# Kernel tuning notes

Hardware: AMD Instinct MI355X
Metric: run time of the kernel (lower is better)

## Reference

```python
import jax, jax.numpy as jnp
import numpy as np

T, N, E = 4, 50000, 800000
F, H, C_HID, C_OUT = 256, 128, 512, 2
SLOPE = 11.0 / 48.0  # torch RReLU eval-mode slope = (1/8 + 1/3) / 2


def _topk_pool(x, scorer, k):
    # x: [N, d], scorer: [d, 1] -> [d, k]
    scores = (x @ scorer) / jnp.maximum(jnp.linalg.norm(scorer), 1e-6)  # [N, 1]
    _, idx = jax.lax.top_k(scores[:, 0], k)
    return (x[idx] * jnp.tanh(scores[idx])).T


def _gru_cell(prev_Q, z, Wu, Uu, bu, Wr, Ur, br, Wh, Uh, bh):
    u = jax.nn.sigmoid(Wu @ z + Uu @ prev_Q + bu)
    r = jax.nn.sigmoid(Wr @ z + Ur @ prev_Q + br)
    h_cap = jnp.tanh(Wh @ z + Uh @ (r * prev_Q) + bh)
    return (1.0 - u) * prev_Q + u * h_cap


def _gcn_conv(x, src, dst, W):
    ones = jnp.ones(src.shape[0], x.dtype)
    deg_out = jnp.clip(jax.ops.segment_sum(ones, src, num_segments=N), 1.0)
    deg_in = jnp.clip(jax.ops.segment_sum(ones, dst, num_segments=N), 1.0)
    h = (x * (deg_out ** -0.5)[:, None]) @ W          # project first (out <= in)
    agg = jax.ops.segment_sum(h[src], dst, num_segments=N)
    out = agg * (deg_in ** -0.5)[:, None]
    return jnp.where(out >= 0, out, SLOPE * out)      # RReLU (eval mode)


def setup_inputs() -> dict:
    key = jax.random.key(0)
    ks = jax.random.split(key, 32)
    s = 0.05
    d = {}
    d['feats'] = jax.random.normal(ks[0], (T, N, F), jnp.float32)
    d['edges'] = jax.random.randint(ks[1], (T, 2, E), 0, N)
    d['scorer0'] = jax.random.normal(ks[2], (F, 1), jnp.float32) * s
    d['scorer1'] = jax.random.normal(ks[3], (H, 1), jnp.float32) * s
    d['gcn_W0'] = jax.random.normal(ks[4], (F, H), jnp.float32) * s
    d['gcn_W1'] = jax.random.normal(ks[5], (H, H), jnp.float32) * s
    i = 6
    for g in ('u', 'r', 'h'):
        d[g + '_W0'] = jax.random.normal(ks[i], (F, F), jnp.float32) * s; i += 1
        d[g + '_U0'] = jax.random.normal(ks[i], (F, F), jnp.float32) * s; i += 1
        d[g + '_b0'] = jax.random.normal(ks[i], (F, H), jnp.float32) * s; i += 1
    for g in ('u', 'r', 'h'):
        d[g + '_W1'] = jax.random.normal(ks[i], (H, H), jnp.float32) * s; i += 1
        d[g + '_U1'] = jax.random.normal(ks[i], (H, H), jnp.float32) * s; i += 1
        d[g + '_b1'] = jax.random.normal(ks[i], (H, H), jnp.float32) * s; i += 1
    d['mlp_W1'] = jax.random.normal(ks[i], (H, C_HID), jnp.float32) * s; i += 1
    d['mlp_b1'] = jax.random.normal(ks[i], (C_HID,), jnp.float32) * s; i += 1
    d['mlp_W2'] = jax.random.normal(ks[i], (C_HID, C_OUT), jnp.float32) * s; i += 1
    d['mlp_b2'] = jax.random.normal(ks[i], (C_OUT,), jnp.float32) * s
    return d


def reference(feats, edges, scorer0, scorer1, gcn_W0, gcn_W1,
              u_W0, u_U0, u_b0, r_W0, r_U0, r_b0, h_W0, h_U0, h_b0,
              u_W1, u_U1, u_b1, r_W1, r_U1, r_b1, h_W1, h_U1, h_b1,
              mlp_W1, mlp_b1, mlp_W2, mlp_b2):
    feat_list = [feats[t] for t in range(T)]
    scorers = [scorer0, scorer1]
    gcn_Ws = [gcn_W0, gcn_W1]
    grus = [(u_W0, u_U0, u_b0, r_W0, r_U0, r_b0, h_W0, h_U0, h_b0),
            (u_W1, u_U1, u_b1, r_W1, r_U1, r_b1, h_W1, h_U1, h_b1)]
    for i in range(2):
        W = gcn_Ws[i]
        for t in range(T):
            src, dst = edges[t, 0], edges[t, 1]
            X_tilde = _topk_pool(feat_list[t], scorers[i], H)
            W = _gru_cell(W, X_tilde, *grus[i])
            feat_list[t] = _gcn_conv(feat_list[t], src, dst, W)
    x = feat_list[-1]
    x = jnp.maximum(x @ mlp_W1 + mlp_b1, 0.0)
    return x @ mlp_W2 + mlp_b2
```

## Files before the change

kernel.cpp:

```cpp
#include <hip/hip_runtime.h>

#define NT 4
#define NN 50000
#define NE 800000
#define FD 256
#define HD 128
#define CH 512
#define NBINS 4096
#define CAPC 256
#define RSLOPE 0.22916666666666666f

#define NCH 32
#define CHE (NE / NCH)
#define HALFN 25000
#define WPH 12500
#define WPC 25000

#define C_NORM0 0
#define C_NORM1 1

#define SCAN_BLOCKS 49
#define BT0SZ (HD * 2 * FD)
#define BT1SZ (HD * 2 * HD)

#define SU_NORM0 0
#define SU_NORM1 1
#define SU_CVT_A 2
#define SU_CVT_B 66
#define SU_CVT_C 98
#define SU_CAT0 114
#define SU_CAT1 1650
#define SU_SPL0 2034
#define SU_SPL1 2290
#define SU_CPQ0 2354
#define SU_CPQ1 2386
#define SU_ZBAR 2402
#define SU_TOTAL 2403

typedef __attribute__((ext_vector_type(8))) short bf16x8;
typedef __attribute__((ext_vector_type(4))) float f32x4;

__device__ __forceinline__ float wsumf(float v) {
  for (int m = 32; m > 0; m >>= 1) v += __shfl_xor(v, m, 64);
  return v;
}

__device__ __forceinline__ unsigned short f2bf(float x) {
  unsigned int u = __float_as_uint(x);
  u += 0x7fffu + ((u >> 16) & 1u);
  return (unsigned short)(u >> 16);
}
__device__ __forceinline__ float bf2f(unsigned short h) {
  return __uint_as_float(((unsigned int)h) << 16);
}
__device__ __forceinline__ int sbin(float s) {
  int b = (int)floorf((s + 16.f) * 128.f);
  return max(0, min(NBINS - 1, b));
}

__device__ __forceinline__ void gbar(unsigned int* bar, int nblk, int gen) {
  __syncthreads();
  if (threadIdx.x == 0) {
    __threadfence();
    atomicAdd(bar, 1u);
    unsigned int tgt = (unsigned int)(nblk * (gen + 1));
    while (atomicAdd(bar, 0u) < tgt) __builtin_amdgcn_s_sleep(2);
    __threadfence();
  }
  __syncthreads();
}

__device__ __forceinline__ void d_norm(const float* s, int d, float* ctlf, int slot,
                                       float* red) {
  float v = ((int)threadIdx.x < d) ? s[threadIdx.x] * s[threadIdx.x] : 0.f;
  red[threadIdx.x] = v;
  __syncthreads();
  for (int o = 128; o > 0; o >>= 1) {
    if ((int)threadIdx.x < o) red[threadIdx.x] += red[threadIdx.x + o];
    __syncthreads();
  }
  if (threadIdx.x == 0) ctlf[slot] = fmaxf(sqrtf(red[0]), 1e-6f);
}

__device__ __forceinline__ void d_cvtT(int bx, int by, const float* __restrict__ src, int C,
                                       unsigned short* __restrict__ dhi,
                                       unsigned short* __restrict__ dlo,
                                       int ldd, int roff, float (*t)[33]) {
  int bc = bx * 32, br = by * 32;
  int lr = threadIdx.x >> 5, lc = threadIdx.x & 31;
#pragma unroll
  for (int q = 0; q < 4; ++q) {
    int r = br + lr + q * 8;
    t[lr + q * 8][lc] = src[(size_t)r * C + bc + lc];
  }
  __syncthreads();
#pragma unroll
  for (int q = 0; q < 4; ++q) {
    int dr = lr + q * 8;
    float v = t[lc][dr];
    unsigned short h = f2bf(v);
    unsigned short l = f2bf(v - bf2f(h));
    size_t o = (size_t)(bc + dr) * ldd + roff + br + lc;
    dhi[o] = h;
    dlo[o] = l;
  }
}

__device__ __forceinline__ void d_catsplit(int blk, int d, const float* __restrict__ Wu,
                                           const float* __restrict__ Uu,
                                           const float* __restrict__ Wr,
                                           const float* __restrict__ Ur,
                                           const float* __restrict__ Wh,
                                           unsigned short* __restrict__ hi,
                                           unsigned short* __restrict__ lo) {
  int idx = blk * 256 + threadIdx.x;
  int K = 2 * d;
  if (idx >= 3 * d * K) return;
  int row = idx / K, col = idx - row * K;
  int reg = row / d;
  int i = row - reg * d;
  float v;
  if (reg == 0) v = (col < d) ? Wu[i * d + col] : Uu[i * d + col - d];
  else if (reg == 1) v = (col < d) ? Wr[i * d + col] : Ur[i * d + col - d];
  else v = (col < d) ? Wh[i * d + col] : 0.f;
  unsigned short h = f2bf(v);
  hi[idx] = h;
  lo[idx] = f2bf(v - bf2f(h));
}

__device__ __forceinline__ void d_split(int blk, int n, const float* __restrict__ src,
                                        unsigned short* __restrict__ hi,
                                        unsigned short* __restrict__ lo) {
  int idx = blk * 256 + threadIdx.x;
  if (idx >= n) return;
  float v = src[idx];
  unsigned short h = f2bf(v);
  hi[idx] = h;
  lo[idx] = f2bf(v - bf2f(h));
}

__global__ __launch_bounds__(256) void k_startup(
    const float* __restrict__ scorer0, const float* __restrict__ scorer1,
    float* __restrict__ ctlf,
    const float* __restrict__ mlpW1, unsigned short* __restrict__ mW1thi,
    unsigned short* __restrict__ mW1tlo,
    const float* __restrict__ gcnW0, const float* __restrict__ gcnW1,
    unsigned short* __restrict__ bt0hi, unsigned short* __restrict__ bt0lo,
    unsigned short* __restrict__ bt1hi, unsigned short* __restrict__ bt1lo,
    const float* __restrict__ u_W0, const float* __restrict__ u_U0,
    const float* __restrict__ r_W0, const float* __restrict__ r_U0,
    const float* __restrict__ h_W0,
    unsigned short* __restrict__ acat0hi, unsigned short* __restrict__ acat0lo,
    const float* __restrict__ u_W1, const float* __restrict__ u_U1,
    const float* __restrict__ r_W1, const float* __restrict__ r_U1,
    const float* __restrict__ h_W1,
    unsigned short* __restrict__ acat1hi, unsigned short* __restrict__ acat1lo,
    const float* __restrict__ uh0, unsigned short* __restrict__ uh0hi,
    unsigned short* __restrict__ uh0lo,
    const float* __restrict__ uh1, unsigned short* __restrict__ uh1hi,
    unsigned short* __restrict__ uh1lo,
    float* __restrict__ Q0, float* __restrict__ Q1,
    unsigned int* __restrict__ bar) {
  __shared__ float red[256];
  __shared__ float tile[32][33];
  int b = blockIdx.x;
  if (b == SU_NORM0) { d_norm(scorer0, FD, ctlf, C_NORM0, red); return; }
  if (b == SU_NORM1) { d_norm(scorer1, HD, ctlf, C_NORM1, red); return; }
  if (b < SU_CVT_B) { int r = b - SU_CVT_A; d_cvtT(r & 15, r >> 4, mlpW1, CH, mW1thi, mW1tlo, HD, 0, tile); return; }
  if (b < SU_CVT_C) { int r = b - SU_CVT_B; d_cvtT(r & 3, r >> 2, gcnW0, HD, bt0hi, bt0lo, 2 * FD, FD, tile); return; }
  if (b < SU_CAT0)  { int r = b - SU_CVT_C; d_cvtT(r & 3, r >> 2, gcnW1, HD, bt1hi, bt1lo, 2 * HD, HD, tile); return; }
  if (b < SU_CAT1)  { d_catsplit(b - SU_CAT0, FD, u_W0, u_U0, r_W0, r_U0, h_W0, acat0hi, acat0lo); return; }
  if (b < SU_SPL0)  { d_catsplit(b - SU_CAT1, HD, u_W1, u_U1, r_W1, r_U1, h_W1, acat1hi, acat1lo); return; }
  if (b < SU_SPL1)  { d_split(b - SU_SPL0, FD * FD, uh0, uh0hi, uh0lo); return; }
  if (b < SU_CPQ0)  { d_split(b - SU_SPL1, HD * HD, uh1, uh1hi, uh1lo); return; }
  if (b < SU_CPQ1)  { int i = (b - SU_CPQ0) * 256 + threadIdx.x; ((float4*)Q0)[i] = ((const float4*)gcnW0)[i]; return; }
  if (b < SU_ZBAR)  { int i = (b - SU_CPQ1) * 256 + threadIdx.x; ((float4*)Q1)[i] = ((const float4*)gcnW1)[i]; return; }
  if (threadIdx.x < 16) bar[threadIdx.x] = 0;
}

__global__ __launch_bounds__(1024) void k_degC(const int* __restrict__ edges,
                                               unsigned int* __restrict__ chist) {
  __shared__ unsigned int lcnt[WPH];
  int t = blockIdx.y, c = blockIdx.x;
  int tid = threadIdx.x;
  for (int dir = 0; dir < 2; ++dir) {
    const int* E = edges + (size_t)t * 2 * NE + (size_t)dir * NE + (size_t)c * CHE;
    for (int half = 0; half < 2; ++half) {
      for (int i = tid; i < WPH; i += 1024) lcnt[i] = 0;
      __syncthreads();
      int lo = half * HALFN;
      for (int j = tid; j < CHE; j += 1024) {
        int n = E[j] - lo;
        if ((unsigned)n < (unsigned)HALFN)
          atomicAdd(&lcnt[n >> 1], 1u << ((n & 1) * 16));
      }
      __syncthreads();
      unsigned int* dst = chist + (((size_t)dir * NT + t) * NCH + c) * WPC + (size_t)half * WPH;
      for (int i = tid; i < WPH; i += 1024) dst[i] = lcnt[i];
      __syncthreads();
    }
  }
}

__global__ __launch_bounds__(1024) void k_scanB(const unsigned int* __restrict__ chist,
                                                unsigned int* __restrict__ lbase,
                                                float* __restrict__ dor4,
                                                float* __restrict__ din4,
                                                int* __restrict__ rowptr4,
                                                int* __restrict__ bsum4) {
  int t = blockIdx.y;
  int tid = threadIdx.x;
  int g = blockIdx.x * 1024 + tid;
  int lane = tid & 63, wid = tid >> 6;
  int v = 0;
  if (g < NN) {
    int w = g >> 1, sh = (g & 1) * 16;
    const unsigned int* oh = chist + ((size_t)0 * NT + t) * NCH * WPC;
    const unsigned int* ih = chist + ((size_t)1 * NT + t) * NCH * WPC;
    int o = 0;
#pragma unroll
    for (int c = 0; c < NCH; ++c) o += (oh[(size_t)c * WPC + w] >> sh) & 0xffff;
    dor4[t * NN + g] = 1.f / sqrtf((float)max(o, 1));
    int run = 0;
#pragma unroll
    for (int c = 0; c < NCH; ++c) {
      lbase[((size_t)t * NCH + c) * NN + g] = (unsigned int)run;
      run += (ih[(size_t)c * WPC + w] >> sh) & 0xffff;
    }
    v = run;
    din4[t * NN + g] = 1.f / sqrtf((float)max(v, 1));
  }
  int s = v;
  for (int o = 1; o < 64; o <<= 1) {
    int u = __shfl_up(s, o, 64);
    if (lane >= o) s += u;
  }
  __shared__ int ws[16];
  if (lane == 63) ws[wid] = s;
  __syncthreads();
  if (wid == 0 && lane < 16) {
    int u = ws[lane];
    int ss = u;
    for (int o = 1; o < 16; o <<= 1) {
      int w2 = __shfl_up(ss, o, 64);
      if (lane >= o) ss += w2;
    }
    ws[lane] = ss - u;
  }
  __syncthreads();
  int incl = s + ws[wid];
  if (g < NN) rowptr4[(size_t)t * (NN + 1) + g] = incl - v;
  if (tid == 1023) bsum4[t * SCAN_BLOCKS + blockIdx.x] = incl;
}

__global__ __launch_bounds__(1024) void k_scan2b(int* __restrict__ rowptr4,
                                                 const int* __restrict__ bsum4) {
  int t = blockIdx.x;
  int* rowptr = rowptr4 + (size_t)t * (NN + 1);
  const int* bsum = bsum4 + t * SCAN_BLOCKS;
  __shared__ int boff[SCAN_BLOCKS];
// ... 77 lines not shown
  __shared__ float stv[HD];
  __shared__ int sidx[HD];
  __shared__ int thrBin, cnt;
  int tid = threadIdx.x;
  for (int i = tid; i < NBINS; i += 1024) hist[i] = 0;
  if (tid == 0) cnt = 0;
  __syncthreads();
  for (int i = tid; i < NN; i += 1024) atomicAdd(&hist[sbin(scores[i])], 1);
  __syncthreads();

  int h0 = hist[4 * tid + 0], h1 = hist[4 * tid + 1];
  int h2 = hist[4 * tid + 2], h3 = hist[4 * tid + 3];
  int l3 = h3, l2 = h2 + l3, l1 = h1 + l2, l0 = h0 + l1;
  sufT[tid] = l0;
  __syncthreads();
  for (int off = 1; off < 1024; off <<= 1) {
    int u = (tid + off < 1024) ? sufT[tid + off] : 0;
    __syncthreads();
    sufT[tid] += u;
    __syncthreads();
  }
  {
    int higher = sufT[tid] - l0;
    int S0 = l0 + higher, S1 = l1 + higher, S2 = l2 + higher, S3 = l3 + higher;
    int S4 = higher;
    if (S3 >= HD && S4 < HD) thrBin = 4 * tid + 3;
    else if (S2 >= HD && S3 < HD) thrBin = 4 * tid + 2;
    else if (S1 >= HD && S2 < HD) thrBin = 4 * tid + 1;
    else if (S0 >= HD && S1 < HD) thrBin = 4 * tid + 0;
  }
  __syncthreads();
  int thr = thrBin;
  for (int i = tid; i < NN; i += 1024) {
    float s = scores[i];
    if (sbin(s) >= thr) {
      int p = atomicAdd(&cnt, 1);
      if (p < CAPC) { cs[p] = s; ci[p] = i; }
    }
  }
  __syncthreads();
  int M = min(cnt, CAPC);
  for (int i = tid; i < CAPC; i += 1024)
    if (i >= M) { cs[i] = -3.4e38f; ci[i] = 0x7fffffff; }
  __syncthreads();
  for (int k = 2; k <= CAPC; k <<= 1) {
    for (int j = k >> 1; j > 0; j >>= 1) {
      int i = tid;
      if (i < CAPC) {
        int l = i ^ j;
        if (l > i) {
          float si = cs[i], sl = cs[l];
          int di = ci[i], dl = ci[l];
          bool lb = (sl > si) || (sl == si && dl < di);
          bool ib = (si > sl) || (si == sl && di < dl);
          bool dir = ((i & k) == 0);
          if (dir ? lb : ib) {
            cs[i] = sl; cs[l] = si; ci[i] = dl; ci[l] = di;
          }
        }
      }
      __syncthreads();
    }
  }
  if (tid < HD) {
    stv[tid] = tanhf(cs[tid]);
    sidx[tid] = ci[tid];
  }
  __syncthreads();
  for (int e4 = tid * 4; e4 < D * HD; e4 += 1024 * 4) {
    int j = e4 >> LOGD, f = e4 & (D - 1);
    float4 x = *(const float4*)&X[(size_t)sidx[j] * D + f];
    float sv = stv[j];
    x.x *= sv; x.y *= sv; x.z *= sv; x.w *= sv;
    ushort4 h, l;
    h.x = f2bf(x.x); l.x = f2bf(x.x - bf2f(h.x));
    h.y = f2bf(x.y); l.y = f2bf(x.y - bf2f(h.y));
    h.z = f2bf(x.z); l.z = f2bf(x.z - bf2f(h.z));
    h.w = f2bf(x.w); l.w = f2bf(x.w - bf2f(h.w));
    *(ushort4*)&bthi[(size_t)j * ldb + f] = h;
    *(ushort4*)&btlo[(size_t)j * ldb + f] = l;
  }
}

__device__ __forceinline__ void gruA_body(
    int bx, const unsigned short* __restrict__ Ahi, const unsigned short* __restrict__ Alo,
    const unsigned short* __restrict__ Bhi, const unsigned short* __restrict__ Blo,
    int d, const float* __restrict__ bu, const float* __restrict__ br,
    const float* __restrict__ bh, const float* __restrict__ Q,
    float* __restrict__ u, float* __restrict__ hz,
    unsigned short* __restrict__ rqThi, unsigned short* __restrict__ rqTlo,
    unsigned short* AshH, unsigned short* AshL,
    unsigned short* BshH, unsigned short* BshL) {
  int K = 2 * d;
  int tid = threadIdx.x;
  int lane = tid & 63, wave = tid >> 6;
  int wr = wave >> 1, wc = wave & 1;
  int n0 = bx * 64;
  f32x4 acc[2][4];
#pragma unroll
  for (int m = 0; m < 2; ++m)
#pragma unroll
    for (int n = 0; n < 4; ++n) acc[m][n] = (f32x4){0.f, 0.f, 0.f, 0.f};
  int arow = tid >> 2, aseg = tid & 3;
  int as = (aseg ^ (arow & 3)) * 8;
  int kseg = lane >> 4;
  for (int k0 = 0; k0 < K; k0 += 32) {
    __syncthreads();
    {
      size_t off = (size_t)(n0 + arow) * K + k0 + aseg * 8;
      *(bf16x8*)&AshH[arow * 32 + as] = *(const bf16x8*)(Ahi + off);
      *(bf16x8*)&AshL[arow * 32 + as] = *(const bf16x8*)(Alo + off);
    }
#pragma unroll
    for (int h = 0; h < 2; ++h) {
      int id = tid + h * 256;
      int br2 = id >> 2, bseg = id & 3;
      int bs = (bseg ^ (br2 & 3)) * 8;
      size_t off = (size_t)br2 * K + k0 + bseg * 8;
      *(bf16x8*)&BshH[br2 * 32 + bs] = *(const bf16x8*)(Bhi + off);
      *(bf16x8*)&BshL[br2 * 32 + bs] = *(const bf16x8*)(Blo + off);
    }
    __syncthreads();
    bf16x8 ah[2], al[2], bh8[4], bl8[4];
#pragma unroll
    for (int m = 0; m < 2; ++m) {
      int row = wr * 32 + m * 16 + (lane & 15);
      int s = (kseg ^ (row & 3)) * 8;
      ah[m] = *(bf16x8*)&AshH[row * 32 + s];
      al[m] = *(bf16x8*)&AshL[row * 32 + s];
    }
#pragma unroll
    for (int n = 0; n < 4; ++n) {
      int col = wc * 64 + n * 16 + (lane & 15);
      int s = (kseg ^ (col & 3)) * 8;
      bh8[n] = *(bf16x8*)&BshH[col * 32 + s];
      bl8[n] = *(bf16x8*)&BshL[col * 32 + s];
    }
#pragma unroll
    for (int m = 0; m < 2; ++m)
#pragma unroll
      for (int n = 0; n < 4; ++n) {
        acc[m][n] = __builtin_amdgcn_mfma_f32_16x16x32_bf16(ah[m], bh8[n], acc[m][n], 0, 0, 0);
        acc[m][n] = __builtin_amdgcn_mfma_f32_16x16x32_bf16(al[m], bh8[n], acc[m][n], 0, 0, 0);
        acc[m][n] = __builtin_amdgcn_mfma_f32_16x16x32_bf16(ah[m], bl8[n], acc[m][n], 0, 0, 0);
      }
  }
  int reg = n0 / d;
#pragma unroll
  for (int m = 0; m < 2; ++m) {
#pragma unroll
    for (int q = 0; q < 4; ++q) {
      int row = n0 + wr * 32 + m * 16 + (lane >> 4) * 4 + q;
      int i = row - reg * d;
#pragma unroll
      for (int n = 0; n < 4; ++n) {
        int col = wc * 64 + n * 16 + (lane & 15);
        float a = acc[m][n][q];
        if (reg == 0) {
          u[i * HD + col] = 1.f / (1.f + expf(-(a + bu[i * HD + col])));
        } else if (reg == 1) {
          float r = 1.f / (1.f + expf(-(a + br[i * HD + col])));
          float rq = r * Q[i * HD + col];
          unsigned short h = f2bf(rq);
          rqThi[(size_t)col * d + i] = h;
          rqTlo[(size_t)col * d + i] = f2bf(rq - bf2f(h));
        } else {
          hz[i * HD + col] = a + bh[i * HD + col];
        }
      }
    }
  }
}

__device__ __forceinline__ void gruB_body(
    int bx, const unsigned short* __restrict__ Ahi, const unsigned short* __restrict__ Alo,
    const unsigned short* __restrict__ Bhi, const unsigned short* __restrict__ Blo,
    int d, const float* __restrict__ hz, const float* __restrict__ u,
    float* __restrict__ Q, unsigned short* __restrict__ BTWhi,
    unsigned short* __restrict__ BTWlo, int ldbt,
    unsigned short* AshH, unsigned short* AshL,
    unsigned short* BshH, unsigned short* BshL) {
  int K = d;
  int tid = threadIdx.x;
  int lane = tid & 63, wave = tid >> 6;
  int wr = wave >> 1, wc = wave & 1;
  int n0 = bx * 64;
  f32x4 acc[2][4];
#pragma unroll
  for (int m = 0; m < 2; ++m)
#pragma unroll
    for (int n = 0; n < 4; ++n) acc[m][n] = (f32x4){0.f, 0.f, 0.f, 0.f};
  int arow = tid >> 2, aseg = tid & 3;
  int as = (aseg ^ (arow & 3)) * 8;
  int kseg = lane >> 4;
  for (int k0 = 0; k0 < K; k0 += 32) {
    __syncthreads();
    {
      size_t off = (size_t)(n0 + arow) * K + k0 + aseg * 8;
      *(bf16x8*)&AshH[arow * 32 + as] = *(const bf16x8*)(Ahi + off);
      *(bf16x8*)&AshL[arow * 32 + as] = *(const bf16x8*)(Alo + off);
    }
#pragma unroll
    for (int h = 0; h < 2; ++h) {
      int id = tid + h * 256;
      int br2 = id >> 2, bseg = id & 3;
      int bs = (bseg ^ (br2 & 3)) * 8;
      size_t off = (size_t)br2 * K + k0 + bseg * 8;
      *(bf16x8*)&BshH[br2 * 32 + bs] = *(const bf16x8*)(Bhi + off);
      *(bf16x8*)&BshL[br2 * 32 + bs] = *(const bf16x8*)(Blo + off);
    }
    __syncthreads();
    bf16x8 ah[2], al[2], bh8[4], bl8[4];
#pragma unroll
    for (int m = 0; m < 2; ++m) {
      int row = wr * 32 + m * 16 + (lane & 15);
      int s = (kseg ^ (row & 3)) * 8;
      ah[m] = *(bf16x8*)&AshH[row * 32 + s];
      al[m] = *(bf16x8*)&AshL[row * 32 + s];
    }
#pragma unroll
    for (int n = 0; n < 4; ++n) {
      int col = wc * 64 + n * 16 + (lane & 15);
      int s = (kseg ^ (col & 3)) * 8;
      bh8[n] = *(bf16x8*)&BshH[col * 32 + s];
      bl8[n] = *(bf16x8*)&BshL[col * 32 + s];
    }
#pragma unroll
    for (int m = 0; m < 2; ++m)
#pragma unroll
      for (int n = 0; n < 4; ++n) {
        acc[m][n] = __builtin_amdgcn_mfma_f32_16x16x32_bf16(ah[m], bh8[n], acc[m][n], 0, 0, 0);
        acc[m][n] = __builtin_amdgcn_mfma_f32_16x16x32_bf16(al[m], bh8[n], acc[m][n], 0, 0, 0);
        acc[m][n] = __builtin_amdgcn_mfma_f32_16x16x32_bf16(ah[m], bl8[n], acc[m][n], 0, 0, 0);
      }
  }
#pragma unroll
  for (int m = 0; m < 2; ++m) {
#pragma unroll
    for (int q = 0; q < 4; ++q) {
      int i = n0 + wr * 32 + m * 16 + (lane >> 4) * 4 + q;
#pragma unroll
      for (int n = 0; n < 4; ++n) {
        int col = wc * 64 + n * 16 + (lane & 15);
        float hc = tanhf(acc[m][n][q] + hz[i * HD + col]);
        float uu = u[i * HD + col];
        float qv = Q[i * HD + col];
        float wn = (1.f - uu) * qv + uu * hc;
        Q[i * HD + col] = wn;
        unsigned short h = f2bf(wn);
        BTWhi[(size_t)col * ldbt + i] = h;
        BTWlo[(size_t)col * ldbt + i] = f2bf(wn - bf2f(h));
      }
    }
  }
}

__global__ __launch_bounds__(256) void k_gruChain(
    const unsigned short* __restrict__ Ahi, const unsigned short* __restrict__ Alo,
    unsigned short* __restrict__ bthi, unsigned short* __restrict__ btlo, long btSz,
    int d, const float* __restrict__ gb_u, const float* __restrict__ gb_r,
    const float* __restrict__ gb_h, float* __restrict__ Q,
    float* __restrict__ ubuf, float* __restrict__ hzbuf,
    unsigned short* __restrict__ rqThi, unsigned short* __restrict__ rqTlo,
    const unsigned short* __restrict__ uhhi, const unsigned short* __restrict__ uhlo,
    unsigned int* bar) {
  __shared__ unsigned short AshH[64 * 32], AshL[64 * 32];
  __shared__ unsigned short BshH[128 * 32], BshL[128 * 32];
  int nb = (int)gridDim.x;
  for (int t = 0; t < NT; ++t) {
    gruA_body((int)blockIdx.x, Ahi, Alo,
              bthi + (size_t)t * btSz, btlo + (size_t)t * btSz, d,
              gb_u, gb_r, gb_h, Q, ubuf, hzbuf, rqThi, rqTlo,
              AshH, AshL, BshH, BshL);
    gbar(bar, nb, 2 * t);
    if ((int)blockIdx.x < (d >> 6)) {
      size_t nxt = (size_t)((t + 1) & 3) * btSz;
      gruB_body((int)blockIdx.x, uhhi, uhlo, rqThi, rqTlo, d, hzbuf, ubuf, Q,
                bthi + nxt + d, btlo + nxt + d, 2 * d,
                AshH, AshL, BshH, BshL);
    }
    if (t < NT - 1) gbar(bar, nb, 2 * t + 1);
  }
}

__global__ __launch_bounds__(256) void k_convL0(
    const float* __restrict__ feats,
    const unsigned short* __restrict__ bt0hi, const unsigned short* __restrict__ bt0lo,
    float* __restrict__ C4, const float* __restrict__ dor4) {
  __shared__ unsigned short AshH[64 * 32], AshL[64 * 32];
  __shared__ unsigned short BshH[128 * 32], BshL[128 * 32];
  const int K = FD, ldb = 2 * FD;
  int t = blockIdx.z;
  const float* Af = feats + (size_t)t * NN * FD;
  size_t bOff = (size_t)((t + 1) & 3) * BT0SZ + FD;
  const unsigned short* Bhi = bt0hi + bOff;
  const unsigned short* Blo = bt0lo + bOff;
  float* C = C4 + (size_t)t * NN * HD;
  const float* rs = dor4 + (size_t)t * NN;
  int tid = threadIdx.x;
  int lane = tid & 63, wave = tid >> 6;
  int wr = wave >> 1, wc = wave & 1;
  int n0 = blockIdx.x * 64;
  f32x4 acc[2][4];
#pragma unroll
  for (int m = 0; m < 2; ++m)
#pragma unroll
    for (int n = 0; n < 4; ++n) acc[m][n] = (f32x4){0.f, 0.f, 0.f, 0.f};

  int arow = tid >> 2, aseg = tid & 3;
  int as = (aseg ^ (arow & 3)) * 8;
  int kseg = lane >> 4;

  for (int k0 = 0; k0 < K; k0 += 32) {
    __syncthreads();
    {
      bf16x8 vh = (bf16x8)(short)0, vl = (bf16x8)(short)0;
      int row = n0 + arow;
      if (row < NN) {
        const float* g = Af + (size_t)row * K + k0 + aseg * 8;
        float4 v0 = *(const float4*)g;
        float4 v1 = *(const float4*)(g + 4);
        float xs[8] = {v0.x, v0.y, v0.z, v0.w, v1.x, v1.y, v1.z, v1.w};
#pragma unroll
        for (int j = 0; j < 8; ++j) {
          unsigned short h = f2bf(xs[j]);
          vh[j] = (short)h;
          vl[j] = (short)f2bf(xs[j] - bf2f(h));
        }
      }
      *(bf16x8*)&AshH[arow * 32 + as] = vh;
      *(bf16x8*)&AshL[arow * 32 + as] = vl;
    }
#pragma unroll
    for (int h = 0; h < 2; ++h) {
      int id = tid + h * 256;
      int br = id >> 2, bseg = id & 3;
      int bs = (bseg ^ (br & 3)) * 8;
      size_t off = (size_t)br * ldb + k0 + bseg * 8;
      *(bf16x8*)&BshH[br * 32 + bs] = *(const bf16x8*)(Bhi + off);
      *(bf16x8*)&BshL[br * 32 + bs] = *(const bf16x8*)(Blo + off);
    }
    __syncthreads();

    bf16x8 ah[2], al[2], bh[4], bl[4];
#pragma unroll
    for (int m = 0; m < 2; ++m) {
      int row = wr * 32 + m * 16 + (lane & 15);
      int s = (kseg ^ (row & 3)) * 8;
      ah[m] = *(bf16x8*)&AshH[row * 32 + s];
      al[m] = *(bf16x8*)&AshL[row * 32 + s];
    }
#pragma unroll
    for (int n = 0; n < 4; ++n) {
      int col = wc * 64 + n * 16 + (lane & 15);
      int s = (kseg ^ (col & 3)) * 8;
      bh[n] = *(bf16x8*)&BshH[col * 32 + s];
      bl[n] = *(bf16x8*)&BshL[col * 32 + s];
    }
#pragma unroll
    for (int m = 0; m < 2; ++m)
#pragma unroll
      for (int n = 0; n < 4; ++n) {
        acc[m][n] = __builtin_amdgcn_mfma_f32_16x16x32_bf16(ah[m], bh[n], acc[m][n], 0, 0, 0);
        acc[m][n] = __builtin_amdgcn_mfma_f32_16x16x32_bf16(al[m], bh[n], acc[m][n], 0, 0, 0);
// ... 279 lines not shown
    float2 v5 = *(const float2*)&h[(size_t)s5 * HD + l2o];
    float2 v6 = *(const float2*)&h[(size_t)s6 * HD + l2o];
    float2 v7 = *(const float2*)&h[(size_t)s7 * HD + l2o];
    ax += ((v0.x + v1.x) + (v2.x + v3.x)) + ((v4.x + v5.x) + (v6.x + v7.x));
    ay += ((v0.y + v1.y) + (v2.y + v3.y)) + ((v4.y + v5.y) + (v6.y + v7.y));
  }
  for (; e + 2 <= end; e += 2) {
    int s0 = srcs[e + 0], s1 = srcs[e + 1];
    float2 v0 = *(const float2*)&h[(size_t)s0 * HD + l2o];
    float2 v1 = *(const float2*)&h[(size_t)s1 * HD + l2o];
    ax += v0.x + v1.x;
    ay += v0.y + v1.y;
  }
  for (; e < end; ++e) {
    int s = srcs[e];
    float2 v = *(const float2*)&h[(size_t)s * HD + l2o];
    ax += v.x; ay += v.y;
  }
  float dn = din4[(size_t)t * NN + w];
  ax *= dn; ay *= dn;
  ax = ax >= 0.f ? ax : RSLOPE * ax;
  ay = ay >= 0.f ? ay : RSLOPE * ay;
  *(float2*)&featA4[((size_t)t * NN + w) * HD + l2o] = make_float2(ax, ay);
  if (t == NT - 1) {
    unsigned short hx = f2bf(ax), hy = f2bf(ay);
    unsigned short lx = f2bf(ax - bf2f(hx)), ly = f2bf(ay - bf2f(hy));
    *(ushort2*)&outHi[(size_t)w * HD + l2o] = make_ushort2(hx, hy);
    *(ushort2*)&outLo[(size_t)w * HD + l2o] = make_ushort2(lx, ly);
  }
  float sp = ax * scorer[l2o] + ay * scorer[l2o + 1];
  sp = wsumf(sp);
  if (lane == 0) scores1_4[(size_t)t * NN + w] = sp / ctlf[C_NORM1];
}

extern "C" void kernel_launch(void* const* d_in, const int* in_sizes, int n_in,
                              void* d_out, int out_size, void* d_ws, size_t ws_size,
                              hipStream_t stream) {
  (void)in_sizes; (void)n_in; (void)out_size; (void)ws_size;
  const float* feats = (const float*)d_in[0];
  const int* edges = (const int*)d_in[1];
  const float* scorer0 = (const float*)d_in[2];
  const float* scorer1 = (const float*)d_in[3];
  const float* gcnW0 = (const float*)d_in[4];
  const float* gcnW1 = (const float*)d_in[5];
  const float* g0[9];
  const float* g1[9];
  for (int i = 0; i < 9; ++i) {
    g0[i] = (const float*)d_in[6 + i];
    g1[i] = (const float*)d_in[15 + i];
  }
  const float* mlpW1 = (const float*)d_in[24];
  const float* mlpB1 = (const float*)d_in[25];
  const float* mlpW2 = (const float*)d_in[26];
  const float* mlpB2 = (const float*)d_in[27];
  float* out = (float*)d_out;

  char* p = (char*)d_ws;
  auto carve = [&p](size_t bytes) {
    void* r = (void*)p;
    p += (bytes + 511) & ~(size_t)511;
    return r;
  };
  float* featA4 = (float*)carve((size_t)NT * NN * HD * 4);
  float* hbuf4  = (float*)carve((size_t)NT * NN * HD * 4);
  unsigned short* fahi = (unsigned short*)carve((size_t)NN * HD * 2);
  unsigned short* falo = (unsigned short*)carve((size_t)NN * HD * 2);
  int* srcs4   = (int*)carve((size_t)NT * NE * 4);
  int* rowptr4 = (int*)carve((size_t)NT * (NN + 1) * 4);
  unsigned int* chist = (unsigned int*)carve((size_t)2 * NT * NCH * WPC * 4);
  unsigned int* lbase = (unsigned int*)carve((size_t)NT * NCH * NN * 4);
  int* bsum4   = (int*)carve((size_t)NT * SCAN_BLOCKS * 4);
  float* dor4  = (float*)carve((size_t)NT * NN * 4);
  float* din4  = (float*)carve((size_t)NT * NN * 4);
  float* scores0 = (float*)carve((size_t)NT * NN * 4);
  float* scores1_4 = (float*)carve((size_t)NT * NN * 4);
  float* ctlf  = (float*)carve(64 * 4);
  unsigned short* bt0hi = (unsigned short*)carve((size_t)NT * BT0SZ * 2);
  unsigned short* bt0lo = (unsigned short*)carve((size_t)NT * BT0SZ * 2);
  unsigned short* bt1hi = (unsigned short*)carve((size_t)NT * BT1SZ * 2);
  unsigned short* bt1lo = (unsigned short*)carve((size_t)NT * BT1SZ * 2);
  unsigned short* rqThi = (unsigned short*)carve((size_t)HD * FD * 2);
  unsigned short* rqTlo = (unsigned short*)carve((size_t)HD * FD * 2);
  float* ubuf_f = (float*)carve((size_t)FD * HD * 4);
  float* hzbuf  = (float*)carve((size_t)FD * HD * 4);
  unsigned short* acat0hi = (unsigned short*)carve((size_t)3 * FD * 2 * FD * 2);
  unsigned short* acat0lo = (unsigned short*)carve((size_t)3 * FD * 2 * FD * 2);
  unsigned short* acat1hi = (unsigned short*)carve((size_t)3 * HD * 2 * HD * 2);
  unsigned short* acat1lo = (unsigned short*)carve((size_t)3 * HD * 2 * HD * 2);
  unsigned short* uh0hi = (unsigned short*)carve((size_t)FD * FD * 2);
  unsigned short* uh0lo = (unsigned short*)carve((size_t)FD * FD * 2);
  unsigned short* uh1hi = (unsigned short*)carve((size_t)HD * HD * 2);
  unsigned short* uh1lo = (unsigned short*)carve((size_t)HD * HD * 2);
  float* Q0 = (float*)carve((size_t)FD * HD * 4);
  float* Q1 = (float*)carve((size_t)HD * HD * 4);
  unsigned short* mW1thi = (unsigned short*)carve((size_t)CH * HD * 2);
  unsigned short* mW1tlo = (unsigned short*)carve((size_t)CH * HD * 2);
  unsigned int* barbuf = (unsigned int*)carve(64 * 4);

  k_startup<<<SU_TOTAL, 256, 0, stream>>>(
      scorer0, scorer1, ctlf, mlpW1, mW1thi, mW1tlo, gcnW0, gcnW1,
      bt0hi, bt0lo, bt1hi, bt1lo,
      g0[0], g0[1], g0[3], g0[4], g0[6], acat0hi, acat0lo,
      g1[0], g1[1], g1[3], g1[4], g1[6], acat1hi, acat1lo,
      g0[7], uh0hi, uh0lo, g1[7], uh1hi, uh1lo, Q0, Q1, barbuf);

  k_scores0_all<<<dim3(12500, NT), 256, 0, stream>>>(feats, scorer0, ctlf, scores0);
  k_degC<<<dim3(NCH, NT), 1024, 0, stream>>>(edges, chist);
  k_scanB<<<dim3(SCAN_BLOCKS, NT), 1024, 0, stream>>>(chist, lbase, dor4, din4, rowptr4, bsum4);
  k_scan2b<<<NT, 1024, 0, stream>>>(rowptr4, bsum4);
  k_scatC<<<dim3(NCH, NT), 1024, 0, stream>>>(edges, rowptr4, lbase, srcs4);
  k_pool<8><<<NT, 1024, 0, stream>>>(feats, (long)NN * FD, scores0, NN,
                                     bt0hi, bt0lo, (long)BT0SZ, 2 * FD);

  k_gruChain<<<3 * FD / 64, 256, 0, stream>>>(
      acat0hi, acat0lo, bt0hi, bt0lo, (long)BT0SZ, FD,
      g0[2], g0[5], g0[8], Q0, ubuf_f, hzbuf, rqThi, rqTlo,
      uh0hi, uh0lo, barbuf + 0);

  const int gM = (NN + 63) / 64;

  k_convL0<<<dim3(gM, 1, NT), 256, 0, stream>>>(feats, bt0hi, bt0lo, hbuf4, dor4);

  k_aggB<<<dim3(12500, NT), 256, 0, stream>>>(hbuf4, rowptr4, srcs4, din4, featA4,
                                              scorer1, ctlf, scores1_4, fahi, falo);

  k_pool<7><<<NT, 1024, 0, stream>>>(featA4, (long)NN * HD, scores1_4, NN,
                                     bt1hi, bt1lo, (long)BT1SZ, 2 * HD);

  k_gruChain<<<3 * HD / 64, 256, 0, stream>>>(
      acat1hi, acat1lo, bt1hi, bt1lo, (long)BT1SZ, HD,
      g1[2], g1[5], g1[8], Q1, ubuf_f, hzbuf, rqThi, rqTlo,
      uh1hi, uh1lo, barbuf + 1);

  k_gemm3<<<dim3(gM, 1), 256, 0, stream>>>(fahi, falo, HD,
                                           bt1hi + HD, bt1lo + HD, 2 * HD,
                                           hbuf4, HD, NN, HD, dor4 + (size_t)3 * NN);
  k_gemmMLPagg<<<gM, 256, 0, stream>>>(hbuf4, rowptr4 + (size_t)3 * (NN + 1),
                                       srcs4 + (size_t)3 * NE, din4 + (size_t)3 * NN,
                                       mW1thi, mW1tlo, mlpB1, mlpW2, mlpB2, out, NN);
}
```

Baseline: 1.126 ms.

## Split GRU chain into parallel W·z precompute and single-block recurrent kernel

The W·z half of every GRU gate product does not depend on the recurrent state, so it is now computed for all timesteps at once in a parallel kernel with the biases folded in. The remaining U·Q recurrence runs in a single 512-thread block, which replaces the grid-wide atomic barriers with __syncthreads. This removes the cross-block spin barriers and the serial per-timestep W·z work. In exchange the recurrent part runs on one block with much less parallelism, and the precomputed wz buffers add extra memory traffic.

```diff
diff --git a/kernel.cpp b/kernel.cpp
--- a/kernel.cpp
+++ b/kernel.cpp
@@ -34,8 +34,7 @@
 #define SU_SPL1 2290
 #define SU_CPQ0 2354
 #define SU_CPQ1 2386
-#define SU_ZBAR 2402
-#define SU_TOTAL 2403
+#define SU_TOTAL 2402
 
 typedef __attribute__((ext_vector_type(8))) short bf16x8;
 typedef __attribute__((ext_vector_type(4))) float f32x4;
@@ -56,18 +55,6 @@
 __device__ __forceinline__ int sbin(float s) {
   int b = (int)floorf((s + 16.f) * 128.f);
   return max(0, min(NBINS - 1, b));
-}
-
-__device__ __forceinline__ void gbar(unsigned int* bar, int nblk, int gen) {
-  __syncthreads();
-  if (threadIdx.x == 0) {
-    __threadfence();
-    atomicAdd(bar, 1u);
-    unsigned int tgt = (unsigned int)(nblk * (gen + 1));
-    while (atomicAdd(bar, 0u) < tgt) __builtin_amdgcn_s_sleep(2);
-    __threadfence();
-  }
-  __syncthreads();
 }
 
 __device__ __forceinline__ void d_norm(const float* s, int d, float* ctlf, int slot,
@@ -145,8 +132,8 @@
     const float* __restrict__ mlpW1, unsigned short* __restrict__ mW1thi,
     unsigned short* __restrict__ mW1tlo,
     const float* __restrict__ gcnW0, const float* __restrict__ gcnW1,
-    unsigned short* __restrict__ bt0hi, unsigned short* __restrict__ bt0lo,
-    unsigned short* __restrict__ bt1hi, unsigned short* __restrict__ bt1lo,
+    unsigned short* __restrict__ qT0hi, unsigned short* __restrict__ qT0lo,
+    unsigned short* __restrict__ qT1hi, unsigned short* __restrict__ qT1lo,
     const float* __restrict__ u_W0, const float* __restrict__ u_U0,
     const float* __restrict__ r_W0, const float* __restrict__ r_U0,
     const float* __restrict__ h_W0,
@@ -159,23 +146,21 @@
     unsigned short* __restrict__ uh0lo,
     const float* __restrict__ uh1, unsigned short* __restrict__ uh1hi,
     unsigned short* __restrict__ uh1lo,
-    float* __restrict__ Q0, float* __restrict__ Q1,
-    unsigned int* __restrict__ bar) {
+    float* __restrict__ Q0, float* __restrict__ Q1) {
   __shared__ float red[256];
   __shared__ float tile[32][33];
   int b = blockIdx.x;
   if (b == SU_NORM0) { d_norm(scorer0, FD, ctlf, C_NORM0, red); return; }
   if (b == SU_NORM1) { d_norm(scorer1, HD, ctlf, C_NORM1, red); return; }
   if (b < SU_CVT_B) { int r = b - SU_CVT_A; d_cvtT(r & 15, r >> 4, mlpW1, CH, mW1thi, mW1tlo, HD, 0, tile); return; }
-  if (b < SU_CVT_C) { int r = b - SU_CVT_B; d_cvtT(r & 3, r >> 2, gcnW0, HD, bt0hi, bt0lo, 2 * FD, FD, tile); return; }
-  if (b < SU_CAT0)  { int r = b - SU_CVT_C; d_cvtT(r & 3, r >> 2, gcnW1, HD, bt1hi, bt1lo, 2 * HD, HD, tile); return; }
+  if (b < SU_CVT_C) { int r = b - SU_CVT_B; d_cvtT(r & 3, r >> 2, gcnW0, HD, qT0hi, qT0lo, FD, 0, tile); return; }
+  if (b < SU_CAT0)  { int r = b - SU_CVT_C; d_cvtT(r & 3, r >> 2, gcnW1, HD, qT1hi, qT1lo, HD, 0, tile); return; }
   if (b < SU_CAT1)  { d_catsplit(b - SU_CAT0, FD, u_W0, u_U0, r_W0, r_U0, h_W0, acat0hi, acat0lo); return; }
   if (b < SU_SPL0)  { d_catsplit(b - SU_CAT1, HD, u_W1, u_U1, r_W1, r_U1, h_W1, acat1hi, acat1lo); return; }
   if (b < SU_SPL1)  { d_split(b - SU_SPL0, FD * FD, uh0, uh0hi, uh0lo); return; }
   if (b < SU_CPQ0)  { d_split(b - SU_SPL1, HD * HD, uh1, uh1hi, uh1lo); return; }
   if (b < SU_CPQ1)  { int i = (b - SU_CPQ0) * 256 + threadIdx.x; ((float4*)Q0)[i] = ((const float4*)gcnW0)[i]; return; }
-  if (b < SU_ZBAR)  { int i = (b - SU_CPQ1) * 256 + threadIdx.x; ((float4*)Q1)[i] = ((const float4*)gcnW1)[i]; return; }
-  if (threadIdx.x < 16) bar[threadIdx.x] = 0;
+  { int i = (b - SU_CPQ1) * 256 + threadIdx.x; ((float4*)Q1)[i] = ((const float4*)gcnW1)[i]; }
 }
 
 __global__ __launch_bounds__(1024) void k_degC(const int* __restrict__ edges,
@@ -419,32 +404,24 @@
   }
 }
 
-__device__ __forceinline__ void gruA_body(
-    int bx, const unsigned short* __restrict__ Ahi, const unsigned short* __restrict__ Alo,
+__device__ __forceinline__ void mm64x128(
+    int tid, int n0,
+    const unsigned short* __restrict__ Ahi, const unsigned short* __restrict__ Alo,
+    int lda, int aoff,
     const unsigned short* __restrict__ Bhi, const unsigned short* __restrict__ Blo,
-    int d, const float* __restrict__ bu, const float* __restrict__ br,
-    const float* __restrict__ bh, const float* __restrict__ Q,
-    float* __restrict__ u, float* __restrict__ hz,
-    unsigned short* __restrict__ rqThi, unsigned short* __restrict__ rqTlo,
+    int ldb, int K,
     unsigned short* AshH, unsigned short* AshL,
-    unsigned short* BshH, unsigned short* BshL) {
-  int K = 2 * d;
-  int tid = threadIdx.x;
+    unsigned short* BshH, unsigned short* BshL,
+    f32x4 (&acc)[2][4]) {
   int lane = tid & 63, wave = tid >> 6;
   int wr = wave >> 1, wc = wave & 1;
-  int n0 = bx * 64;
-  f32x4 acc[2][4];
-#pragma unroll
-  for (int m = 0; m < 2; ++m)
-#pragma unroll
-    for (int n = 0; n < 4; ++n) acc[m][n] = (f32x4){0.f, 0.f, 0.f, 0.f};
   int arow = tid >> 2, aseg = tid & 3;
   int as = (aseg ^ (arow & 3)) * 8;
   int kseg = lane >> 4;
   for (int k0 = 0; k0 < K; k0 += 32) {
     __syncthreads();
     {
-      size_t off = (size_t)(n0 + arow) * K + k0 + aseg * 8;
+      size_t off = (size_t)(n0 + arow) * lda + aoff + k0 + aseg * 8;
       *(bf16x8*)&AshH[arow * 32 + as] = *(const bf16x8*)(Ahi + off);
       *(bf16x8*)&AshL[arow * 32 + as] = *(const bf16x8*)(Alo + off);
     }
@@ -453,7 +430,7 @@
       int id = tid + h * 256;
       int br2 = id >> 2, bseg = id & 3;
       int bs = (bseg ^ (br2 & 3)) * 8;
-      size_t off = (size_t)br2 * K + k0 + bseg * 8;
+      size_t off = (size_t)br2 * ldb + k0 + bseg * 8;
       *(bf16x8*)&BshH[br2 * 32 + bs] = *(const bf16x8*)(Bhi + off);
       *(bf16x8*)&BshL[br2 * 32 + bs] = *(const bf16x8*)(Blo + off);
     }
@@ -482,7 +459,32 @@
         acc[m][n] = __builtin_amdgcn_mfma_f32_16x16x32_bf16(ah[m], bl8[n], acc[m][n], 0, 0, 0);
       }
   }
+}
+
+__global__ __launch_bounds__(256) void k_wz(
+    const unsigned short* __restrict__ Ahi, const unsigned short* __restrict__ Alo,
+    const unsigned short* __restrict__ bthi, const unsigned short* __restrict__ btlo,
+    long btSz, int d,
+    const float* __restrict__ bu, const float* __restrict__ br,
+    const float* __restrict__ bh, float* __restrict__ wz) {
+  __shared__ unsigned short AshH[64 * 32], AshL[64 * 32];
+  __shared__ unsigned short BshH[128 * 32], BshL[128 * 32];
+  int t = blockIdx.z;
+  int tid = threadIdx.x;
+  int lane = tid & 63, wave = tid >> 6;
+  int wr = wave >> 1, wc = wave & 1;
+  int n0 = blockIdx.x * 64;
+  f32x4 acc[2][4];
+#pragma unroll
+  for (int m = 0; m < 2; ++m)
+#pragma unroll
+    for (int n = 0; n < 4; ++n) acc[m][n] = (f32x4){0.f, 0.f, 0.f, 0.f};
+  mm64x128(tid, n0, Ahi, Alo, 2 * d, 0,
+           bthi + (size_t)t * btSz, btlo + (size_t)t * btSz, 2 * d, d,
+           AshH, AshL, BshH, BshL, acc);
   int reg = n0 / d;
+  const float* bias = (reg == 0) ? bu : (reg == 1) ? br : bh;
+  float* wzt = wz + (size_t)t * 3 * d * HD;
 #pragma unroll
   for (int m = 0; m < 2; ++m) {
 #pragma unroll
@@ -492,131 +494,95 @@
 #pragma unroll
       for (int n = 0; n < 4; ++n) {
         int col = wc * 64 + n * 16 + (lane & 15);
-        float a = acc[m][n][q];
-        if (reg == 0) {
-          u[i * HD + col] = 1.f / (1.f + expf(-(a + bu[i * HD + col])));
-        } else if (reg == 1) {
-          float r = 1.f / (1.f + expf(-(a + br[i * HD + col])));
-          float rq = r * Q[i * HD + col];
-          unsigned short h = f2bf(rq);
-          rqThi[(size_t)col * d + i] = h;
-          rqTlo[(size_t)col * d + i] = f2bf(rq - bf2f(h));
-        } else {
-          hz[i * HD + col] = a + bh[i * HD + col];
-        }
-      }
-    }
-  }
-}
-
-__device__ __forceinline__ void gruB_body(
-    int bx, const unsigned short* __restrict__ Ahi, const unsigned short* __restrict__ Alo,
-    const unsigned short* __restrict__ Bhi, const unsigned short* __restrict__ Blo,
-    int d, const float* __restrict__ hz, const float* __restrict__ u,
-    float* __restrict__ Q, unsigned short* __restrict__ BTWhi,
-    unsigned short* __restrict__ BTWlo, int ldbt,
-    unsigned short* AshH, unsigned short* AshL,
-    unsigned short* BshH, unsigned short* BshL) {
-  int K = d;
-  int tid = threadIdx.x;
+        wzt[(size_t)row * HD + col] = acc[m][n][q] + bias[i * HD + col];
+      }
+    }
+  }
+}
+
+__global__ __launch_bounds__(512) void k_gruR(
+    const unsigned short* __restrict__ Ahi, const unsigned short* __restrict__ Alo,
+    const unsigned short* __restrict__ uhhi, const unsigned short* __restrict__ uhlo,
+    const float* __restrict__ wz, float* __restrict__ Q,
+    unsigned short* __restrict__ qThi, unsigned short* __restrict__ qTlo,
+    unsigned short* __restrict__ bthi, unsigned short* __restrict__ btlo,
+    long btSz, int d, float* __restrict__ ubuf,
+    unsigned short* __restrict__ rqThi, unsigned short* __restrict__ rqTlo) {
+  __shared__ unsigned short AshH[2][64 * 32], AshL[2][64 * 32];
+  __shared__ unsigned short BshH[2][128 * 32], BshL[2][128 * 32];
+  int tid = (int)threadIdx.x & 255, sub = (int)threadIdx.x >> 8;
   int lane = tid & 63, wave = tid >> 6;
   int wr = wave >> 1, wc = wave & 1;
-  int n0 = bx * 64;
-  f32x4 acc[2][4];
-#pragma unroll
-  for (int m = 0; m < 2; ++m)
-#pragma unroll
-    for (int n = 0; n < 4; ++n) acc[m][n] = (f32x4){0.f, 0.f, 0.f, 0.f};
-  int arow = tid >> 2, aseg = tid & 3;
-  int as = (aseg ^ (arow & 3)) * 8;
-  int kseg = lane >> 4;
-  for (int k0 = 0; k0 < K; k0 += 32) {
-    __syncthreads();
-    {
-      size_t off = (size_t)(n0 + arow) * K + k0 + aseg * 8;
-      *(bf16x8*)&AshH[arow * 32 + as] = *(const bf16x8*)(Ahi + off);
-      *(bf16x8*)&AshL[arow * 32 + as] = *(const bf16x8*)(Alo + off);
-    }
-#pragma unroll
-    for (int h = 0; h < 2; ++h) {
-      int id = tid + h * 256;
-      int br2 = id >> 2, bseg = id & 3;
-      int bs = (bseg ^ (br2 & 3)) * 8;
-      size_t off = (size_t)br2 * K + k0 + bseg * 8;
-      *(bf16x8*)&BshH[br2 * 32 + bs] = *(const bf16x8*)(Bhi + off);
-      *(bf16x8*)&BshL[br2 * 32 + bs] = *(const bf16x8*)(Blo + off);
-    }
-    __syncthreads();
-    bf16x8 ah[2], al[2], bh8[4], bl8[4];
-#pragma unroll
-    for (int m = 0; m < 2; ++m) {
-      int row = wr * 32 + m * 16 + (lane & 15);
-      int s = (kseg ^ (row & 3)) * 8;
-      ah[m] = *(bf16x8*)&AshH[row * 32 + s];
-      al[m] = *(bf16x8*)&AshL[row * 32 + s];
-    }
-#pragma unroll
-    for (int n = 0; n < 4; ++n) {
-      int col = wc * 64 + n * 16 + (lane & 15);
-      int s = (kseg ^ (col & 3)) * 8;
-      bh8[n] = *(bf16x8*)&BshH[col * 32 + s];
-      bl8[n] = *(bf16x8*)&BshL[col * 32 + s];
-    }
-#pragma unroll
-    for (int m = 0; m < 2; ++m)
-#pragma unroll
-      for (int n = 0; n < 4; ++n) {
-        acc[m][n] = __builtin_amdgcn_mfma_f32_16x16x32_bf16(ah[m], bh8[n], acc[m][n], 0, 0, 0);
-        acc[m][n] = __builtin_amdgcn_mfma_f32_16x16x32_bf16(al[m], bh8[n], acc[m][n], 0, 0, 0);
-        acc[m][n] = __builtin_amdgcn_mfma_f32_16x16x32_bf16(ah[m], bl8[n], acc[m][n], 0, 0, 0);
-      }
-  }
-#pragma unroll
-  for (int m = 0; m < 2; ++m) {
-#pragma unroll
-    for (int q = 0; q < 4; ++q) {
-      int i = n0 + wr * 32 + m * 16 + (lane >> 4) * 4 + q;
-#pragma unroll
-      for (int n = 0; n < 4; ++n) {
-        int col = wc * 64 + n * 16 + (lane & 15);
-        float hc = tanhf(acc[m][n][q] + hz[i * HD + col]);
-        float uu = u[i * HD + col];
-        float qv = Q[i * HD + col];
-        float wn = (1.f - uu) * qv + uu * hc;
-        Q[i * HD + col] = wn;
-        unsigned short h = f2bf(wn);
-        BTWhi[(size_t)col * ldbt + i] = h;
-        BTWlo[(size_t)col * ldbt + i] = f2bf(wn - bf2f(h));
-      }
-    }
-  }
-}
-
-__global__ __launch_bounds__(256) void k_gruChain(
-    const unsigned short* __restrict__ Ahi, const unsigned short* __restrict__ Alo,
-    unsigned short* __restrict__ bthi, unsigned short* __restrict__ btlo, long btSz,
-    int d, const float* __restrict__ gb_u, const float* __restrict__ gb_r,
-    const float* __restrict__ gb_h, float* __restrict__ Q,
-    float* __restrict__ ubuf, float* __restrict__ hzbuf,
-    unsigned short* __restrict__ rqThi, unsigned short* __restrict__ rqTlo,
-    const unsigned short* __restrict__ uhhi, const unsigned short* __restrict__ uhlo,
-    unsigned int* bar) {
-  __shared__ unsigned short AshH[64 * 32], AshL[64 * 32];
-  __shared__ unsigned short BshH[128 * 32], BshL[128 * 32];
-  int nb = (int)gridDim.x;
   for (int t = 0; t < NT; ++t) {
-    gruA_body((int)blockIdx.x, Ahi, Alo,
-              bthi + (size_t)t * btSz, btlo + (size_t)t * btSz, d,
-              gb_u, gb_r, gb_h, Q, ubuf, hzbuf, rqThi, rqTlo,
-              AshH, AshL, BshH, BshL);
-    gbar(bar, nb, 2 * t);
-    if ((int)blockIdx.x < (d >> 6)) {
-      size_t nxt = (size_t)((t + 1) & 3) * btSz;
-      gruB_body((int)blockIdx.x, uhhi, uhlo, rqThi, rqTlo, d, hzbuf, ubuf, Q,
-                bthi + nxt + d, btlo + nxt + d, 2 * d,
-                AshH, AshL, BshH, BshL);
-    }
-    if (t < NT - 1) gbar(bar, nb, 2 * t + 1);
+    const float* wzt = wz + (size_t)t * 3 * d * HD;
+    for (int it = 0; it < (d >> 6); ++it) {
+      int n0 = (sub + 2 * it) * 64;
+      f32x4 acc[2][4];
+#pragma unroll
+      for (int m = 0; m < 2; ++m)
+#pragma unroll
+        for (int n = 0; n < 4; ++n) acc[m][n] = (f32x4){0.f, 0.f, 0.f, 0.f};
+      mm64x128(tid, n0, Ahi, Alo, 2 * d, d, qThi, qTlo, d, d,
+               AshH[sub], AshL[sub], BshH[sub], BshL[sub], acc);
+      int reg = n0 / d;
+#pragma unroll
+      for (int m = 0; m < 2; ++m) {
+#pragma unroll
+        for (int q = 0; q < 4; ++q) {
+          int row = n0 + wr * 32 + m * 16 + (lane >> 4) * 4 + q;
+#pragma unroll
+          for (int n = 0; n < 4; ++n) {
+            int col = wc * 64 + n * 16 + (lane & 15);
+            float a = acc[m][n][q] + wzt[(size_t)row * HD + col];
+            if (reg == 0) {
+              ubuf[row * HD + col] = 1.f / (1.f + expf(-a));
+            } else {
+              int i = row - d;
+              float r = 1.f / (1.f + expf(-a));
+              float rq = r * Q[i * HD + col];
+              unsigned short h = f2bf(rq);
+              rqThi[(size_t)col * d + i] = h;
+              rqTlo[(size_t)col * d + i] = f2bf(rq - bf2f(h));
+            }
+          }
+        }
+      }
+    }
+    __syncthreads();
+    size_t nxt = (size_t)((t + 1) & 3) * btSz;
+    for (int it = 0; it < (d >> 7); ++it) {
+      int n0 = (sub + 2 * it) * 64;
+      f32x4 acc[2][4];
+#pragma unroll
+      for (int m = 0; m < 2; ++m)
+#pragma unroll
+        for (int n = 0; n < 4; ++n) acc[m][n] = (f32x4){0.f, 0.f, 0.f, 0.f};
+      mm64x128(tid, n0, uhhi, uhlo, d, 0, rqThi, rqTlo, d, d,
+               AshH[sub], AshL[sub], BshH[sub], BshL[sub], acc);
+#pragma unroll
+      for (int m = 0; m < 2; ++m) {
+#pragma unroll
+        for (int q = 0; q < 4; ++q) {
+          int i = n0 + wr * 32 + m * 16 + (lane >> 4) * 4 + q;
+#pragma unroll
+          for (int n = 0; n < 4; ++n) {
+            int col = wc * 64 + n * 16 + (lane & 15);
+            float hc = tanhf(acc[m][n][q] + wzt[(size_t)(2 * d + i) * HD + col]);
+            float uu = ubuf[i * HD + col];
+            float qv = Q[i * HD + col];
+            float wn = (1.f - uu) * qv + uu * hc;
+            Q[i * HD + col] = wn;
+            unsigned short h = f2bf(wn);
+            unsigned short l = f2bf(wn - bf2f(h));
+            qThi[(size_t)col * d + i] = h;
+            qTlo[(size_t)col * d + i] = l;
+            bthi[nxt + (size_t)col * 2 * d + d + i] = h;
+            btlo[nxt + (size_t)col * 2 * d + d + i] = l;
+          }
+        }
+      }
+    }
+    __syncthreads();
   }
 }
 
@@ -1062,7 +1028,12 @@
   unsigned short* rqThi = (unsigned short*)carve((size_t)HD * FD * 2);
   unsigned short* rqTlo = (unsigned short*)carve((size_t)HD * FD * 2);
   float* ubuf_f = (float*)carve((size_t)FD * HD * 4);
-  float* hzbuf  = (float*)carve((size_t)FD * HD * 4);
+  float* wz0 = (float*)carve((size_t)NT * 3 * FD * HD * 4);
+  float* wz1 = (float*)carve((size_t)NT * 3 * HD * HD * 4);
+  unsigned short* qT0hi = (unsigned short*)carve((size_t)HD * FD * 2);
+  unsigned short* qT0lo = (unsigned short*)carve((size_t)HD * FD * 2);
+  unsigned short* qT1hi = (unsigned short*)carve((size_t)HD * HD * 2);
+  unsigned short* qT1lo = (unsigned short*)carve((size_t)HD * HD * 2);
   unsigned short* acat0hi = (unsigned short*)carve((size_t)3 * FD * 2 * FD * 2);
   unsigned short* acat0lo = (unsigned short*)carve((size_t)3 * FD * 2 * FD * 2);
   unsigned short* acat1hi = (unsigned short*)carve((size_t)3 * HD * 2 * HD * 2);
@@ -1075,14 +1046,13 @@
   float* Q1 = (float*)carve((size_t)HD * HD * 4);
   unsigned short* mW1thi = (unsigned short*)carve((size_t)CH * HD * 2);
   unsigned short* mW1tlo = (unsigned short*)carve((size_t)CH * HD * 2);
-  unsigned int* barbuf = (unsigned int*)carve(64 * 4);
 
   k_startup<<<SU_TOTAL, 256, 0, stream>>>(
       scorer0, scorer1, ctlf, mlpW1, mW1thi, mW1tlo, gcnW0, gcnW1,
-      bt0hi, bt0lo, bt1hi, bt1lo,
+      qT0hi, qT0lo, qT1hi, qT1lo,
       g0[0], g0[1], g0[3], g0[4], g0[6], acat0hi, acat0lo,
       g1[0], g1[1], g1[3], g1[4], g1[6], acat1hi, acat1lo,
-      g0[7], uh0hi, uh0lo, g1[7], uh1hi, uh1lo, Q0, Q1, barbuf);
+      g0[7], uh0hi, uh0lo, g1[7], uh1hi, uh1lo, Q0, Q1);
 
   k_scores0_all<<<dim3(12500, NT), 256, 0, stream>>>(feats, scorer0, ctlf, scores0);
   k_degC<<<dim3(NCH, NT), 1024, 0, stream>>>(edges, chist);
@@ -1092,10 +1062,11 @@
   k_pool<8><<<NT, 1024, 0, stream>>>(feats, (long)NN * FD, scores0, NN,
                                      bt0hi, bt0lo, (long)BT0SZ, 2 * FD);
 
-  k_gruChain<<<3 * FD / 64, 256, 0, stream>>>(
-      acat0hi, acat0lo, bt0hi, bt0lo, (long)BT0SZ, FD,
-      g0[2], g0[5], g0[8], Q0, ubuf_f, hzbuf, rqThi, rqTlo,
-      uh0hi, uh0lo, barbuf + 0);
+  k_wz<<<dim3(3 * FD / 64, 1, NT), 256, 0, stream>>>(
+      acat0hi, acat0lo, bt0hi, bt0lo, (long)BT0SZ, FD, g0[2], g0[5], g0[8], wz0);
+  k_gruR<<<1, 512, 0, stream>>>(
+      acat0hi, acat0lo, uh0hi, uh0lo, wz0, Q0, qT0hi, qT0lo,
+      bt0hi, bt0lo, (long)BT0SZ, FD, ubuf_f, rqThi, rqTlo);
 
   const int gM = (NN + 63) / 64;
 
@@ -1107,10 +1078,11 @@
   k_pool<7><<<NT, 1024, 0, stream>>>(featA4, (long)NN * HD, scores1_4, NN,
                                      bt1hi, bt1lo, (long)BT1SZ, 2 * HD);
 
-  k_gruChain<<<3 * HD / 64, 256, 0, stream>>>(
-      acat1hi, acat1lo, bt1hi, bt1lo, (long)BT1SZ, HD,
-      g1[2], g1[5], g1[8], Q1, ubuf_f, hzbuf, rqThi, rqTlo,
-      uh1hi, uh1lo, barbuf + 1);
+  k_wz<<<dim3(3 * HD / 64, 1, NT), 256, 0, stream>>>(
+      acat1hi, acat1lo, bt1hi, bt1lo, (long)BT1SZ, HD, g1[2], g1[5], g1[8], wz1);
+  k_gruR<<<1, 512, 0, stream>>>(
+      acat1hi, acat1lo, uh1hi, uh1lo, wz1, Q1, qT1hi, qT1lo,
+      bt1hi, bt1lo, (long)BT1SZ, HD, ubuf_f, rqThi, rqTlo);
 
   k_gemm3<<<dim3(gM, 1), 256, 0, stream>>>(fahi, falo, HD,
                                            bt1hi + HD, bt1lo + HD, 2 * HD,
```

Result: slower. 1.839 ms (+63.4%).
